# Performance work log

Hardware: AMD Instinct MI355X
Metric: run time of the kernel (lower is better)

The kernel has to match this reference:

```python
import jax, jax.numpy as jnp
import numpy as np

V = 50000   # vocab
E = 512     # embedding_dim
H = 512     # hidden_dim
HD = 256    # hidden per direction = H // 2
L = 2       # num_layers
B = 64      # batch
T = 256     # sequence_length
K = 7       # tagset size
START, STOP = 5, 6
NEG = -10000.0


def setup_inputs() -> dict:
    key = jax.random.key(0)
    ks = jax.random.split(key, 12)
    sentence = jax.random.randint(ks[0], (T, B), 0, V)          # [T, B] token ids
    emb = jax.random.normal(ks[1], (V, E), jnp.float32) * 0.02  # embedding table
    # PyTorch LSTM params, stacked: [layer, direction, ...]; gate order i,f,g,o
    w_ih = jax.random.normal(ks[2], (L, 2, 4 * HD, E), jnp.float32) * 0.05
    w_hh = jax.random.normal(ks[3], (L, 2, 4 * HD, HD), jnp.float32) * 0.05
    b_ih = jax.random.normal(ks[4], (L, 2, 4 * HD), jnp.float32) * 0.05
    b_hh = jax.random.normal(ks[5], (L, 2, 4 * HD), jnp.float32) * 0.05
    w_out = jax.random.normal(ks[6], (K, H), jnp.float32) * 0.05  # hidden2tag
    b_out = jax.random.normal(ks[7], (K,), jnp.float32) * 0.05
    trans = jax.random.normal(ks[8], (K, K), jnp.float32)
    trans = trans.at[START, :].set(NEG).at[:, STOP].set(NEG)      # CRF transitions[next, prev]
    h0 = jax.random.normal(ks[9], (2 * L, B, HD), jnp.float32)    # random init hidden, as in module
    c0 = jax.random.normal(ks[10], (2 * L, B, HD), jnp.float32)
    return dict(sentence=sentence, emb=emb, w_ih=w_ih, w_hh=w_hh, b_ih=b_ih,
                b_hh=b_hh, w_out=w_out, b_out=b_out, trans=trans, h0=h0, c0=c0)


def _lstm_dir(x, w_ih_d, w_hh_d, b_ih_d, b_hh_d, h0_d, c0_d, reverse):
    # x: [T, B, in]; returns hidden sequence [T, B, HD]
    xg = jnp.einsum('tbe,ge->tbg', x, w_ih_d) + b_ih_d + b_hh_d  # precompute input gates

    def step(carry, g_t):
        h, c = carry
        g = g_t + h @ w_hh_d.T
        i, f, gg, o = jnp.split(g, 4, axis=-1)
        i = jax.nn.sigmoid(i); f = jax.nn.sigmoid(f)
        gg = jnp.tanh(gg);     o = jax.nn.sigmoid(o)
        c = f * c + i * gg
        h = o * jnp.tanh(c)
        return (h, c), h

    _, hs = jax.lax.scan(step, (h0_d, c0_d), xg, reverse=reverse)
    return hs


def _bilstm_feats(sentence, emb, w_ih, w_hh, b_ih, b_hh, w_out, b_out, h0, c0):
    x = emb[sentence]  # [T, B, E]
    for l in range(L):
        hf = _lstm_dir(x, w_ih[l, 0], w_hh[l, 0], b_ih[l, 0], b_hh[l, 0], h0[2 * l], c0[2 * l], False)
        hb = _lstm_dir(x, w_ih[l, 1], w_hh[l, 1], b_ih[l, 1], b_hh[l, 1], h0[2 * l + 1], c0[2 * l + 1], True)
        x = jnp.concatenate([hf, hb], axis=-1)  # [T, B, H]
    return x @ w_out.T + b_out  # [T, B, K]


def _viterbi(feats, trans):
    # feats: [T, B, K]; vectorized over batch (original looped per sequence)
    v0 = jnp.full((B, K), NEG, feats.dtype).at[:, START].set(0.0)

    def step(v, feat_t):
        sc = v[:, None, :] + trans[None, :, :]   # [B, next, prev]
        bp = jnp.argmax(sc, axis=2)              # [B, K]
        v2 = jnp.max(sc, axis=2) + feat_t
        return v2, bp

    v, bps = jax.lax.scan(step, v0, feats)       # bps: [T, B, K]
    term = v + trans[STOP][None, :]
    last = jnp.argmax(term, axis=1)              # [B]
    score = jnp.max(term, axis=1)                # [B] path score

    def back(tag, bp_t):
        prev = jnp.take_along_axis(bp_t, tag[:, None], axis=1)[:, 0]
        return prev, tag

    _, path = jax.lax.scan(back, last, bps, reverse=True)  # [T, B]
    return path.T.astype(jnp.int32), score


def reference(sentence, emb, w_ih, w_hh, b_ih, b_hh, w_out, b_out, trans, h0, c0):
    feats = _bilstm_feats(sentence, emb, w_ih, w_hh, b_ih, b_hh, w_out, b_out, h0, c0)
    best_path, path_score = _viterbi(feats, trans)
    return best_path, path_score
```

## Files before the change

### kernel.cpp

```cpp
#include <hip/hip_runtime.h>
#include <stdint.h>

#define T_LEN 256
#define BATCH 64
#define EDIM  512
#define HDIM  256
#define GDIM  1024
#define KTAG  7
#define NEGV  -10000.0f

using u16 = unsigned short;
using u32 = unsigned int;
using u64 = unsigned long long;

typedef short    bf16x8 __attribute__((ext_vector_type(8)));
typedef float    f32x4  __attribute__((ext_vector_type(4)));

__device__ __forceinline__ float bflo(u32 u) { return __uint_as_float(u << 16); }
__device__ __forceinline__ float bfhi(u32 u) { return __uint_as_float(u & 0xffff0000u); }
__device__ __forceinline__ float bf2f(u16 u) { return __uint_as_float(((u32)u) << 16); }
__device__ __forceinline__ u16 f2bf(float f) {
    u32 x = __float_as_uint(f);
    u32 r = x + 0x7fffu + ((x >> 16) & 1u);
    return (u16)(r >> 16);
}
__device__ __forceinline__ u32 pack2(float a, float b) {
    return (u32)f2bf(a) | ((u32)f2bf(b) << 16);
}
__device__ __forceinline__ float fsig(float x)  { return __builtin_amdgcn_rcpf(1.f + __expf(-x)); }
__device__ __forceinline__ float ftanh(float x) { return 1.f - 2.f * __builtin_amdgcn_rcpf(1.f + __expf(2.f * x)); }

__device__ __forceinline__ int dot4i8(int a, int b, int c) {
#if __has_builtin(__builtin_amdgcn_sdot4)
    return __builtin_amdgcn_sdot4(a, b, c, false);
#else
    c += (int)(signed char)(a & 0xff)         * (int)(signed char)(b & 0xff);
    c += (int)(signed char)((a >> 8) & 0xff)  * (int)(signed char)((b >> 8) & 0xff);
    c += (int)(signed char)((a >> 16) & 0xff) * (int)(signed char)((b >> 16) & 0xff);
    c += (int)(signed char)(a >> 24)          * (int)(signed char)(b >> 24);
    return c;
#endif
}

__device__ __forceinline__ void bar_lds() {
    asm volatile("s_waitcnt lgkmcnt(0)" ::: "memory");
    __builtin_amdgcn_s_barrier();
    asm volatile("" ::: "memory");
}

__device__ __forceinline__ void gload_lds16(const void* g, void* l) {
    __builtin_amdgcn_global_load_lds((const __attribute__((address_space(1))) u32*)g,
                                     (__attribute__((address_space(3))) u32*)l, 16, 0, 0);
}

__global__ __launch_bounds__(64) void embed_k(const int* __restrict__ sent,
                                              const float* __restrict__ emb,
                                              u16* __restrict__ X) {
    int tb = blockIdx.x;
    int tok = sent[tb];
    const float4* src = (const float4*)(emb + (size_t)tok * EDIM);
    float4 a = src[threadIdx.x * 2];
    float4 b = src[threadIdx.x * 2 + 1];
    uint4 o;
    o.x = pack2(a.x, a.y); o.y = pack2(a.z, a.w);
    o.z = pack2(b.x, b.y); o.w = pack2(b.z, b.w);
    ((uint4*)(X + (size_t)tb * EDIM))[threadIdx.x] = o;
}

__global__ __launch_bounds__(256) void conv_wih(const float* __restrict__ W,
                                                u16* __restrict__ WB) {
    int g = blockIdx.x * 256 + threadIdx.x;
    const float4* src = (const float4*)(W + (size_t)g * 8);
    float4 a = src[0], b = src[1];
    uint4 o;
    o.x = pack2(a.x, a.y); o.y = pack2(a.z, a.w);
    o.z = pack2(b.x, b.y); o.w = pack2(b.z, b.w);
    *(uint4*)(WB + (size_t)g * 8) = o;
}

__global__ __launch_bounds__(256) void repack_whh_i8(const float* __restrict__ Whh,
                                                     uint4* __restrict__ WQ,
                                                     float* __restrict__ SCL) {
    int g  = blockIdx.x * 256 + threadIdx.x;
    int ld = g >> 10, row = g & 1023;
    const float* src = Whh + ((size_t)ld * GDIM + row) * HDIM;
    float m = 1e-30f;
    for (int k4 = 0; k4 < 64; ++k4) {
        float4 w = ((const float4*)src)[k4];
        m = fmaxf(m, fmaxf(fmaxf(fabsf(w.x), fabsf(w.y)), fmaxf(fabsf(w.z), fabsf(w.w))));
    }
    float inv = 127.f / m;
    SCL[ld * GDIM + row] = m / 127.f;
    int r = row >> 8, j = row & 255;
    for (int c8 = 0; c8 < 16; ++c8) {
        u32 dw[4];
        #pragma unroll
        for (int d4 = 0; d4 < 4; ++d4) {
            u32 p = 0;
            #pragma unroll
            for (int bb = 0; bb < 4; ++bb) {
                float w = src[c8 * 16 + d4 * 4 + bb];
                int q = (int)rintf(w * inv);
                q = q > 127 ? 127 : (q < -127 ? -127 : q);
                p |= ((u32)(q & 0xff)) << (8 * bb);
            }
            dw[d4] = p;
        }
        WQ[(size_t)(((ld * 4 + r) * 16 + c8) * 256 + j)] =
            (uint4){dw[0], dw[1], dw[2], dw[3]};
    }
}

__global__ __launch_bounds__(256, 2) void gemm_xg(const u16* __restrict__ A,
                                                  const u16* __restrict__ W,
                                                  const float* __restrict__ Bih,
                                                  const float* __restrict__ Bhh,
                                                  u16* __restrict__ XG) {
    const int d    = blockIdx.z;
    const int brow = blockIdx.x;
    const int bcol = blockIdx.y;
    const int tid  = threadIdx.x;
    const int lane = tid & 63;
    const int wv   = tid >> 6;
    const int l15  = lane & 15;
    const int quad = lane >> 4;
    const int wr   = wv >> 1, wc = wv & 1;

    __shared__ u16 As[2][128 * 64];
    __shared__ u16 Bs[2][128 * 64];

    const u16* Wd = W + (size_t)d * GDIM * EDIM;
    const int srow = tid >> 3;
    const int scol = (tid & 7) * 8;
    const u16* ga = A  + (size_t)(brow * 128 + srow) * EDIM + scol;
    const u16* gb = Wd + (size_t)(bcol * 128 + srow) * EDIM + scol;
    const int loff = srow * 64 + scol;

    f32x4 acc[4][4];
    #pragma unroll
    for (int mt = 0; mt < 4; ++mt)
        #pragma unroll
        for (int nt = 0; nt < 4; ++nt)
            acc[mt][nt] = (f32x4){0.f, 0.f, 0.f, 0.f};

    #pragma unroll
    for (int it = 0; it < 4; ++it) {
        gload_lds16(ga + (size_t)(it * 32) * EDIM, &As[0][loff + it * 32 * 64]);
        gload_lds16(gb + (size_t)(it * 32) * EDIM, &Bs[0][loff + it * 32 * 64]);
    }
    __syncthreads();

    int cur = 0;
    for (int t = 0; t < 8; ++t) {
        if (t < 7) {
            int k0 = (t + 1) * 64;
            #pragma unroll
            for (int it = 0; it < 4; ++it) {
                gload_lds16(ga + (size_t)(it * 32) * EDIM + k0, &As[cur ^ 1][loff + it * 32 * 64]);
                gload_lds16(gb + (size_t)(it * 32) * EDIM + k0, &Bs[cur ^ 1][loff + it * 32 * 64]);
            }
        }
        const u16* Ab = As[cur];
        const u16* Bb = Bs[cur];
        #pragma unroll
        for (int ks = 0; ks < 2; ++ks) {
            bf16x8 av[4], bv[4];
            #pragma unroll
            for (int mt = 0; mt < 4; ++mt)
                av[mt] = *(const bf16x8*)(Ab + (wr * 64 + mt * 16 + l15) * 64 + ks * 32 + quad * 8);
            #pragma unroll
            for (int nt = 0; nt < 4; ++nt)
                bv[nt] = *(const bf16x8*)(Bb + (wc * 64 + nt * 16 + l15) * 64 + ks * 32 + quad * 8);
            #pragma unroll
            for (int mt = 0; mt < 4; ++mt)
                #pragma unroll
                for (int nt = 0; nt < 4; ++nt)
                    acc[mt][nt] = __builtin_amdgcn_mfma_f32_16x16x32_bf16(av[mt], bv[nt], acc[mt][nt], 0, 0, 0);
        }
        __syncthreads();
        cur ^= 1;
    }

    u16* xgd = XG + (size_t)d * ((size_t)16384 * GDIM);
    #pragma unroll
    for (int nt = 0; nt < 4; ++nt) {
        int col = bcol * 128 + wc * 64 + nt * 16 + l15;
        float bias = Bih[d * GDIM + col] + Bhh[d * GDIM + col];
        #pragma unroll
        for (int mt = 0; mt < 4; ++mt) {
            int row0 = brow * 128 + wr * 64 + mt * 16 + quad * 4;
            #pragma unroll
            for (int r = 0; r < 4; ++r)
                xgd[(size_t)(row0 + r) * GDIM + col] = f2bf(acc[mt][nt][r] + bias);
        }
    }
}

__global__ __attribute__((amdgpu_waves_per_eu(4, 4))) __launch_bounds__(1024)
void lstm_scan_i8(
        const u16* __restrict__ XG,
        const uint4* __restrict__ WQ,
        const float* __restrict__ SCL,
        const float* __restrict__ H0,
        const float* __restrict__ C0,
        u16* __restrict__ XOUT) {
    const int b   = blockIdx.x & 63;
    const int d   = blockIdx.x >> 6;
    const int tid = threadIdx.x;
    const int j   = tid & 255;
    const int q   = tid >> 8;

    __shared__ uint4  hq[2][16];
    __shared__ float4 psv[4 * 256];

    uint4 Wr[4][4];
    #pragma unroll
    for (int r = 0; r < 4; ++r)
        #pragma unroll
        for (int c = 0; c < 4; ++c)
            Wr[r][c] = WQ[(size_t)(((d * 4 + r) * 16 + q * 4 + c) * 256 + j)];

    float scl0 = 0.f, scl1 = 0.f, scl2 = 0.f, scl3 = 0.f, cst = 0.f;
    if (q == 0) {
        scl0 = SCL[d * GDIM + 0 * 256 + j];
        scl1 = SCL[d * GDIM + 1 * 256 + j];
        scl2 = SCL[d * GDIM + 2 * 256 + j];
        scl3 = SCL[d * GDIM + 3 * 256 + j];
        float h0v = H0[((size_t)d * BATCH + b) * HDIM + j];
        cst       = C0[((size_t)d * BATCH + b) * HDIM + j];
        int qz = (int)rintf(h0v * 31.75f);
        qz = qz > 127 ? 127 : (qz < -127 ? -127 : qz);
        ((signed char*)hq)[j] = (signed char)qz;
    }
    __syncthreads();

    const u16* xgp = XG + (size_t)d * ((size_t)16384 * GDIM) + (size_t)b * GDIM + j;
    u16 xe[4], xo[4];
    if (q == 0) {
        int t0 = d ? T_LEN - 1 : 0;
        int t1 = d ? T_LEN - 2 : 1;
        #pragma unroll
        for (int r = 0; r < 4; ++r) xe[r] = xgp[(size_t)t0 * (BATCH * GDIM) + r * 256];
        #pragma unroll
        for (int r = 0; r < 4; ++r) xo[r] = xgp[(size_t)t1 * (BATCH * GDIM) + r * 256];
    }

    float hs = 4.f / 127.f;

#define SCAN_SUBSTEP(S, XA, RB, WB)                                                     \
    {                                                                                   \
        const int t_ = d ? (T_LEN - 1 - (S)) : (S);                                     \
        const uint4* hb = (const uint4*)hq + (RB) * 16 + q * 4;                         \
        uint4 hv[4];                                                                    \
        _Pragma("unroll")                                                               \
        for (int c = 0; c < 4; ++c) hv[c] = hb[c];          \
        int a0 = 0, a1 = 0, a2 = 0, a3 = 0;                                             \
        _Pragma("unroll")                                                               \
        for (int c = 0; c < 4; ++c) {                                                   \
            a0 = dot4i8(Wr[0][c].x, hv[c].x, a0);                                       \
            a0 = dot4i8(Wr[0][c].y, hv[c].y, a0);                                       \
            a0 = dot4i8(Wr[0][c].z, hv[c].z, a0);                                       \
            a0 = dot4i8(Wr[0][c].w, hv[c].w, a0);                                       \
            a1 = dot4i8(Wr[1][c].x, hv[c].x, a1);                                       \
            a1 = dot4i8(Wr[1][c].y, hv[c].y, a1);                                       \
            a1 = dot4i8(Wr[1][c].z, hv[c].z, a1);                                       \
            a1 = dot4i8(Wr[1][c].w, hv[c].w, a1);                                       \
            a2 = dot4i8(Wr[2][c].x, hv[c].x, a2);                                       \
            a2 = dot4i8(Wr[2][c].y, hv[c].y, a2);                                       \
            a2 = dot4i8(Wr[2][c].z, hv[c].z, a2);                                       \
            a2 = dot4i8(Wr[2][c].w, hv[c].w, a2);                                       \
            a3 = dot4i8(Wr[3][c].x, hv[c].x, a3);                                       \
            a3 = dot4i8(Wr[3][c].y, hv[c].y, a3);                                       \
            a3 = dot4i8(Wr[3][c].z, hv[c].z, a3);                                       \
            a3 = dot4i8(Wr[3][c].w, hv[c].w, a3);                                       \
        }                                                                               \
             \
        psv[q * 256 + j] = (float4){(float)a0, (float)a1, (float)a2, (float)a3};        \
        bar_lds();                                                                      \
        if (q == 0) {                                                                   \
            float4 p0 = psv[j], p1 = psv[256 + j], p2 = psv[512 + j], p3 = psv[768 + j];\
            float g0 = bf2f(XA[0]) + (p0.x + p1.x + p2.x + p3.x) * (scl0 * hs);         \
            float g1 = bf2f(XA[1]) + (p0.y + p1.y + p2.y + p3.y) * (scl1 * hs);         \
            float g2 = bf2f(XA[2]) + (p0.z + p1.z + p2.z + p3.z) * (scl2 * hs);         \
            float g3 = bf2f(XA[3]) + (p0.w + p1.w + p2.w + p3.w) * (scl3 * hs);         \
            float iv = fsig(g0), fv = fsig(g1), gv = ftanh(g2), ov = fsig(g3);          \
            cst = fv * cst + iv * gv;                                                   \
            float h = ov * ftanh(cst);                                                  \
            XOUT[((size_t)t_ * BATCH + b) * EDIM + d * HDIM + j] = f2bf(h);             \
            int qz = (int)rintf(h * 127.f);                     \
            qz = qz > 127 ? 127 : (qz < -127 ? -127 : qz);                              \
            ((signed char*)hq)[(WB) * 256 + j] = (signed char)qz;                       \
            int s2 = ((S) + 2 < T_LEN) ? (S) + 2 : T_LEN - 1;                           \
            int t2 = d ? (T_LEN - 1 - s2) : s2;                                         \
            _Pragma("unroll")                                                           \
            for (int r = 0; r < 4; ++r)                                                 \
                XA[r] = xgp[(size_t)t2 * (BATCH * GDIM) + r * 256];                     \
        }                                                                               \
        bar_lds();                                                                      \
        hs = 1.f / 127.f;                                                               \
    }

    for (int s = 0; s < T_LEN; s += 2) {
        SCAN_SUBSTEP(s,     xe, 0, 1);
        SCAN_SUBSTEP(s + 1, xo, 1, 0);
    }
#undef SCAN_SUBSTEP
}

__global__ __launch_bounds__(64) void feats_k(const u16* __restrict__ X,
                                              const float* __restrict__ Wout,
                                              const float* __restrict__ Bout,
                                              float* __restrict__ F) {
    int tb = blockIdx.x, lane = threadIdx.x;
    uint4 xv = ((const uint4*)(X + (size_t)tb * EDIM))[lane];
    float xf[8];
    xf[0] = bflo(xv.x); xf[1] = bfhi(xv.x); xf[2] = bflo(xv.y); xf[3] = bfhi(xv.y);
    xf[4] = bflo(xv.z); xf[5] = bfhi(xv.z); xf[6] = bflo(xv.w); xf[7] = bfhi(xv.w);
    #pragma unroll
    for (int k = 0; k < KTAG; ++k) {
        const float4* wpo = (const float4*)(Wout + (size_t)k * EDIM) + lane * 2;
        float4 wa = wpo[0], wb = wpo[1];
        float p = 0.0f;
        p = fmaf(xf[0], wa.x, p); p = fmaf(xf[1], wa.y, p);
        p = fmaf(xf[2], wa.z, p); p = fmaf(xf[3], wa.w, p);
        p = fmaf(xf[4], wb.x, p); p = fmaf(xf[5], wb.y, p);
        p = fmaf(xf[6], wb.z, p); p = fmaf(xf[7], wb.w, p);
        #pragma unroll
        for (int off = 32; off > 0; off >>= 1) p += __shfl_xor(p, off, 64);
        if (lane == 0) F[tb * 8 + k] = p + Bout[k];
    }
}

__global__ __launch_bounds__(64) void viterbi_k(const float* __restrict__ F,
                                                const float* __restrict__ Trans,
                                                u64* __restrict__ BP8,
                                                float* __restrict__ OUT) {
    int b = threadIdx.x;
    float tr[KTAG][KTAG];
    #pragma unroll
    for (int n = 0; n < KTAG; ++n)
        #pragma unroll
        for (int p = 0; p < KTAG; ++p)
            tr[n][p] = Trans[n * KTAG + p];

    float v[KTAG];
    #pragma unroll
    for (int k = 0; k < KTAG; ++k) v[k] = (k == 5) ? 0.0f : NEGV;

    float cf[KTAG], nf[KTAG];
    #pragma unroll
    for (int n = 0; n < KTAG; ++n) cf[n] = F[b * 8 + n];

    for (int t = 0; t < T_LEN; ++t) {
        int tp = (t + 1 < T_LEN) ? t + 1 : t;
        #pragma unroll
        for (int n = 0; n < KTAG; ++n) nf[n] = F[((tp)*BATCH + b) * 8 + n];

        u64 pk = 0;
        float nv[KTAG];
        #pragma unroll
        for (int n = 0; n < KTAG; ++n) {
            float best = v[0] + tr[n][0]; int bi = 0;
            #pragma unroll
            for (int p = 1; p < KTAG; ++p) {
                float s = v[p] + tr[n][p];
                if (s > best) { best = s; bi = p; }
            }
            pk |= ((u64)bi) << (8 * n);
            nv[n] = best + cf[n];
        }
        BP8[t * BATCH + b] = pk;
        #pragma unroll
        for (int n = 0; n < KTAG; ++n) { v[n] = nv[n]; cf[n] = nf[n]; }
    }
    float bs = v[0] + tr[6][0]; int tag = 0;
    #pragma unroll
    for (int k = 1; k < KTAG; ++k) {
        float s = v[k] + tr[6][k];
        if (s > bs) { bs = s; tag = k; }
    }
    OUT[T_LEN * BATCH + b] = bs;
    for (int t = T_LEN - 1; t >= 0; --t) {
        OUT[(size_t)b * T_LEN + t] = (float)tag;
        tag = (int)((BP8[t * BATCH + b] >> (8 * tag)) & 0xff);
    }
}

extern "C" void kernel_launch(void* const* d_in, const int* in_sizes, int n_in,
                              void* d_out, int out_size, void* d_ws, size_t ws_size,
                              hipStream_t stream) {
    const int*   sent  = (const int*)d_in[0];
    const float* emb   = (const float*)d_in[1];
    const float* w_ih  = (const float*)d_in[2];
    const float* w_hh  = (const float*)d_in[3];
    const float* b_ih  = (const float*)d_in[4];
    const float* b_hh  = (const float*)d_in[5];
    const float* w_out = (const float*)d_in[6];
    const float* b_out = (const float*)d_in[7];
    const float* trans = (const float*)d_in[8];
    const float* h0    = (const float*)d_in[9];
    const float* c0    = (const float*)d_in[10];
    float* out = (float*)d_out;

    char* ws = (char*)d_ws;
    u16*   xg    = (u16*)(ws);
    u16*   x     = (u16*)(ws + 67108864);
    u16*   wihB  = (u16*)(ws + 83886080);
    uint4* wq    = (uint4*)(ws + 88080384);
    float* scl   = (float*)(ws + 89128960);
    float* feats = (float*)(ws + 89145344);
    u64*   bp8   = (u64*)(ws + 89669632);

    embed_k<<<16384, 64, 0, stream>>>(sent, emb, x);
    conv_wih<<<1024, 256, 0, stream>>>(w_ih, wihB);
    repack_whh_i8<<<16, 256, 0, stream>>>(w_hh, wq, scl);

    for (int l = 0; l < 2; ++l) {
        gemm_xg<<<dim3(128, 8, 2), 256, 0, stream>>>(
            x, wihB + (size_t)l * 2 * GDIM * EDIM,
            b_ih + (size_t)l * 2 * GDIM, b_hh + (size_t)l * 2 * GDIM, xg);
        lstm_scan_i8<<<128, 1024, 0, stream>>>(
            xg, wq + (size_t)l * 32768, scl + (size_t)l * 2048,
            h0 + (size_t)l * 2 * BATCH * HDIM, c0 + (size_t)l * 2 * BATCH * HDIM, x);
    }

    feats_k<<<16384, 64, 0, stream>>>(x, w_out, b_out, feats);
    viterbi_k<<<1, 64, 0, stream>>>(feats, trans, bp8, out);
}
```

Before: 936.1 us.

## Deepen GEMM prefetch with explicit vmcnt waits, drop waves_per_eu, transpose Viterbi backpointers

The input-gate GEMM now issues two K-tiles ahead and uses explicit s_waitcnt vmcnt/lgkmcnt plus raw barriers instead of __syncthreads. This lets global-to-LDS loads overlap more fully with the MFMA work. The amdgpu_waves_per_eu(4,4) hint on the LSTM scan kernel is removed, which changes the compiler's register budget for the recurrent loop. Viterbi backpointers are stored in a batch-major layout, so each thread's backtrace reads consecutive addresses. The hand-tuned vmcnt count depends on the exact number of loads per stage, and dropping the occupancy hint could change register allocation or cause spills in the scan.

```diff
diff --git a/kernel.cpp b/kernel.cpp
--- a/kernel.cpp
+++ b/kernel.cpp
@@ -136,6 +136,14 @@
     const u16* gb = Wd + (size_t)(bcol * 128 + srow) * EDIM + scol;
     const int loff = srow * 64 + scol;
 
+#define STAGE(buf, kt)                                                              \
+    { int k0_ = (kt) * 64;                                                          \
+      _Pragma("unroll")                                                             \
+      for (int it = 0; it < 4; ++it) {                                              \
+          gload_lds16(ga + (size_t)(it * 32) * EDIM + k0_, &As[buf][loff + it * 32 * 64]); \
+          gload_lds16(gb + (size_t)(it * 32) * EDIM + k0_, &Bs[buf][loff + it * 32 * 64]); \
+      } }
+
     f32x4 acc[4][4];
     #pragma unroll
     for (int mt = 0; mt < 4; ++mt)
@@ -143,25 +151,16 @@
         for (int nt = 0; nt < 4; ++nt)
             acc[mt][nt] = (f32x4){0.f, 0.f, 0.f, 0.f};
 
-    #pragma unroll
-    for (int it = 0; it < 4; ++it) {
-        gload_lds16(ga + (size_t)(it * 32) * EDIM, &As[0][loff + it * 32 * 64]);
-        gload_lds16(gb + (size_t)(it * 32) * EDIM, &Bs[0][loff + it * 32 * 64]);
-    }
-    __syncthreads();
-
-    int cur = 0;
+    STAGE(0, 0);
+    STAGE(1, 1);
+
     for (int t = 0; t < 8; ++t) {
-        if (t < 7) {
-            int k0 = (t + 1) * 64;
-            #pragma unroll
-            for (int it = 0; it < 4; ++it) {
-                gload_lds16(ga + (size_t)(it * 32) * EDIM + k0, &As[cur ^ 1][loff + it * 32 * 64]);
-                gload_lds16(gb + (size_t)(it * 32) * EDIM + k0, &Bs[cur ^ 1][loff + it * 32 * 64]);
-            }
-        }
-        const u16* Ab = As[cur];
-        const u16* Bb = Bs[cur];
+        if (t < 7) { asm volatile("s_waitcnt vmcnt(8)" ::: "memory"); }
+        else       { asm volatile("s_waitcnt vmcnt(0)" ::: "memory"); }
+        __builtin_amdgcn_s_barrier();
+
+        const u16* Ab = As[t & 1];
+        const u16* Bb = Bs[t & 1];
         #pragma unroll
         for (int ks = 0; ks < 2; ++ks) {
             bf16x8 av[4], bv[4];
@@ -177,9 +176,12 @@
                 for (int nt = 0; nt < 4; ++nt)
                     acc[mt][nt] = __builtin_amdgcn_mfma_f32_16x16x32_bf16(av[mt], bv[nt], acc[mt][nt], 0, 0, 0);
         }
-        __syncthreads();
-        cur ^= 1;
-    }
+
+        asm volatile("s_waitcnt lgkmcnt(0)" ::: "memory");
+        __builtin_amdgcn_s_barrier();
+        if (t < 6) STAGE(t & 1, t + 2);
+    }
+#undef STAGE
 
     u16* xgd = XG + (size_t)d * ((size_t)16384 * GDIM);
     #pragma unroll
@@ -196,8 +198,7 @@
     }
 }
 
-__global__ __attribute__((amdgpu_waves_per_eu(4, 4))) __launch_bounds__(1024)
-void lstm_scan_i8(
+__global__ __launch_bounds__(1024) void lstm_scan_i8(
         const u16* __restrict__ XG,
         const uint4* __restrict__ WQ,
         const float* __restrict__ SCL,
@@ -333,7 +334,7 @@
 
 __global__ __launch_bounds__(64) void viterbi_k(const float* __restrict__ F,
                                                 const float* __restrict__ Trans,
-                                                u64* __restrict__ BP8,
+                                                u64* __restrict__ BPT,
                                                 float* __restrict__ OUT) {
     int b = threadIdx.x;
     float tr[KTAG][KTAG];
@@ -369,7 +370,7 @@
             pk |= ((u64)bi) << (8 * n);
             nv[n] = best + cf[n];
         }
-        BP8[t * BATCH + b] = pk;
+        BPT[(b << 8) | t] = pk;
         #pragma unroll
         for (int n = 0; n < KTAG; ++n) { v[n] = nv[n]; cf[n] = nf[n]; }
     }
@@ -382,7 +383,7 @@
     OUT[T_LEN * BATCH + b] = bs;
     for (int t = T_LEN - 1; t >= 0; --t) {
         OUT[(size_t)b * T_LEN + t] = (float)tag;
-        tag = (int)((BP8[t * BATCH + b] >> (8 * tag)) & 0xff);
+        tag = (int)((BPT[(b << 8) | t] >> (8 * tag)) & 0xff);
     }
 }
 
@@ -409,7 +410,7 @@
     uint4* wq    = (uint4*)(ws + 88080384);
     float* scl   = (float*)(ws + 89128960);
     float* feats = (float*)(ws + 89145344);
-    u64*   bp8   = (u64*)(ws + 89669632);
+    u64*   bpt   = (u64*)(ws + 89669632);
 
     embed_k<<<16384, 64, 0, stream>>>(sent, emb, x);
     conv_wih<<<1024, 256, 0, stream>>>(w_ih, wihB);
@@ -425,5 +426,5 @@
     }
 
     feats_k<<<16384, 64, 0, stream>>>(x, w_out, b_out, feats);
-    viterbi_k<<<1, 64, 0, stream>>>(feats, trans, bp8, out);
-}
+    viterbi_k<<<1, 64, 0, stream>>>(feats, trans, bpt, out);
+}
```

New measurement: 897.4 us. 1.04x faster.
